# Performance work log

Hardware: AMD Instinct MI355X
Metric: run time of the kernel (lower is better)

Reference implementation:

```python
import jax, jax.numpy as jnp
import numpy as np

B, N, DEG = 128, 512, 16          # graphs, nodes/graph, avg degree
NB = B * N                        # 65536 nodes
E = NB * DEG                      # 1048576 edges
K1, K2, K3 = 410, 205, 103        # ceil(0.8*512), ceil(0.5*410), ceil(0.5*205)
H, C = 4, 32                      # GAT heads, head dim
F_IN, ED = 128, 7


def _glorot(key, shape, fan_in):
    return jax.random.normal(key, shape, dtype=jnp.float32) / np.float32(np.sqrt(fan_in))


def setup_inputs() -> dict:
    key = jax.random.key(0)
    ks = jax.random.split(key, 24)
    x = jax.random.normal(ks[0], (NB, F_IN), dtype=jnp.float32)
    # random intra-graph edges, then offset per graph
    src = jax.random.randint(ks[1], (E,), 0, N)
    dst = jax.random.randint(ks[2], (E,), 0, N)
    off = jnp.repeat(jnp.arange(B) * N, N * DEG)
    edge_index = jnp.stack([src + off, dst + off]).astype(jnp.int32)
    edge_attr = jax.random.normal(ks[3], (E, ED), dtype=jnp.float32)
    p = {
        'c1_wl': _glorot(ks[4], (F_IN, F_IN), F_IN), 'c1_bl': jnp.zeros((F_IN,), jnp.float32), 'c1_wr': _glorot(ks[5], (F_IN, F_IN), F_IN),
        'p1_w': _glorot(ks[6], (F_IN,), F_IN),
        'c2_wl': _glorot(ks[7], (F_IN, F_IN), F_IN), 'c2_bl': jnp.zeros((F_IN,), jnp.float32), 'c2_wr': _glorot(ks[8], (F_IN, F_IN), F_IN),
        'p2_wrel': _glorot(ks[9], (F_IN, 1), F_IN), 'p2_brel': jnp.zeros((1,), jnp.float32), 'p2_wroot': _glorot(ks[10], (F_IN, 1), F_IN),
        'g_w': _glorot(ks[11], (F_IN, H * C), F_IN), 'g_as': _glorot(ks[12], (H, C), C), 'g_ad': _glorot(ks[13], (H, C), C),
        'g_we': _glorot(ks[14], (ED, H * C), ED), 'g_ae': _glorot(ks[15], (H, C), C), 'g_b': jnp.zeros((H * C,), jnp.float32),
        'p3_wrel': _glorot(ks[16], (F_IN, 1), F_IN), 'p3_brel': jnp.zeros((1,), jnp.float32), 'p3_wroot': _glorot(ks[17], (F_IN, 1), F_IN),
        'l1_w': _glorot(ks[18], (F_IN, F_IN), F_IN), 'l1_b': jnp.zeros((F_IN,), jnp.float32),
        'l2_w': _glorot(ks[19], (F_IN, 64), F_IN), 'l2_b': jnp.zeros((64,), jnp.float32),
        'l3_w': _glorot(ks[20], (64, 1), 64), 'l3_b': jnp.zeros((1,), jnp.float32),
    }
    return {'x': x, 'edge_index': edge_index, 'edge_attr': edge_attr, **p}


def _sage(x, src, dst, emf, wl, bl, wr):
    # SAGEConv: mean-aggregate neighbors (masked edges), lin_l(agg)+lin_r(x)
    agg = jax.ops.segment_sum(x[src] * emf[:, None], dst, num_segments=NB)
    cnt = jax.ops.segment_sum(emf, dst, num_segments=NB)
    mean = agg / jnp.maximum(cnt, 1.0)[:, None]
    return mean @ wl + bl + x @ wr


def _graphconv(x, src, dst, emf, wrel, brel, wroot):
    # GraphConv (SAGPooling score GNN): add-aggregation
    agg = jax.ops.segment_sum(x[src] * emf[:, None], dst, num_segments=NB)
    return (agg @ wrel + brel + x @ wroot).reshape(-1)


def _pool(x, score, nmask, K):
    # per-graph static top-k (equal-size graphs) == PyG topk + filter
    masked = jnp.where(nmask, score, -jnp.inf).reshape(B, N)
    idx = jax.lax.top_k(masked, K)[1]
    nm = jnp.zeros((B, N), dtype=bool).at[jnp.arange(B)[:, None], idx].set(True).reshape(-1)
    x = jnp.where(nm[:, None], x * score[:, None], 0.0)
    return x, nm


def _gap(x, K):
    # global mean pool; dropped nodes are exactly zero, K live nodes per graph
    return x.reshape(B, N, F_IN).sum(axis=1) / K


def _gat(x, src, dst, emf, nmask, edge_attr, w, a_s, a_d, w_e, a_e, b):
    xs = (x @ w).reshape(NB, H, C)
    al_s = (xs * a_s).sum(-1)                                   # [NB,H]
    al_d = (xs * a_d).sum(-1)
    al_e = ((edge_attr @ w_e).reshape(E, H, C) * a_e).sum(-1)    # [E,H]
    alpha = jax.nn.leaky_relu(al_s[src] + al_d[dst] + al_e, 0.2)
    alpha = jnp.where(emf[:, None] > 0, alpha, -jnp.inf)
    # PyG add_self_loops=True with fill_value='mean' for edge_attr
    ea_mean = (edge_attr * emf[:, None]).sum(0) / jnp.maximum(emf.sum(), 1.0)
    al_se = ((ea_mean @ w_e).reshape(H, C) * a_e).sum(-1)        # [H]
    alpha_self = jax.nn.leaky_relu(al_s + al_d + al_se[None, :], 0.2)
    alpha_self = jnp.where(nmask[:, None], alpha_self, -jnp.inf)
    m = jnp.maximum(jax.ops.segment_max(alpha, dst, num_segments=NB), alpha_self)
    m = jnp.where(jnp.isfinite(m), m, 0.0)
    ex = jnp.exp(alpha - m[dst]) * emf[:, None]
    ex_s = jnp.where(nmask[:, None], jnp.exp(alpha_self - m), 0.0)
    den = jnp.maximum(jax.ops.segment_sum(ex, dst, num_segments=NB) + ex_s, 1e-16)
    num = jax.ops.segment_sum(ex[:, :, None] * xs[src], dst, num_segments=NB) + ex_s[:, :, None] * xs
    return (num / den[:, :, None]).reshape(NB, H * C) + b


def _forward(x, edge_index, edge_attr, c1_wl, c1_bl, c1_wr, p1_w, c2_wl, c2_bl, c2_wr,
             p2_wrel, p2_brel, p2_wroot, g_w, g_as, g_ad, g_we, g_ae, g_b,
             p3_wrel, p3_brel, p3_wroot, l1_w, l1_b, l2_w, l2_b, l3_w, l3_b):
    src, dst = edge_index[0], edge_index[1]
    nmask = jnp.ones((NB,), dtype=bool)
    emf = jnp.ones((E,), jnp.float32)

    # block 1: SAGEConv -> TopKPooling(0.8) -> gap
    x = jax.nn.relu(_sage(x, src, dst, emf, c1_wl, c1_bl, c1_wr))
    s1 = jnp.tanh((x @ p1_w) / jnp.linalg.norm(p1_w))
    x, nmask = _pool(x, s1, nmask, K1)
    emf = emf * nmask[src] * nmask[dst]
    x1 = _gap(x, K1)

    # block 2: SAGEConv -> SAGPooling(0.5) -> gap
    x = jax.nn.relu(_sage(x, src, dst, emf, c2_wl, c2_bl, c2_wr))
    s2 = jnp.tanh(_graphconv(x, src, dst, emf, p2_wrel, p2_brel, p2_wroot))
    x, nmask = _pool(x, s2, nmask, K2)
    emf = emf * nmask[src] * nmask[dst]
    x2 = _gap(x, K2)

    # block 3: GATConv(128->32x4, edge_dim=7) -> SAGPooling(0.5) -> gap
    x = jax.nn.relu(_gat(x, src, dst, emf, nmask, edge_attr, g_w, g_as, g_ad, g_we, g_ae, g_b))
    s3 = jnp.tanh(_graphconv(x, src, dst, emf, p3_wrel, p3_brel, p3_wroot))
    x, nmask = _pool(x, s3, nmask, K3)
    x3 = _gap(x, K3)

    h = x1 + x2 + x3
    h = jax.nn.relu(h @ l1_w + l1_b)
    h = jax.nn.relu(h @ l2_w + l2_b)   # dropout identity in eval
    return jax.nn.sigmoid(h @ l3_w + l3_b)[:, 0]


def reference(x, edge_index, edge_attr, c1_wl, c1_bl, c1_wr, p1_w, c2_wl, c2_bl, c2_wr,
              p2_wrel, p2_brel, p2_wroot, g_w, g_as, g_ad, g_we, g_ae, g_b,
              p3_wrel, p3_brel, p3_wroot, l1_w, l1_b, l2_w, l2_b, l3_w, l3_b):
    return _forward(x, edge_index, edge_attr, c1_wl, c1_bl, c1_wr, p1_w, c2_wl, c2_bl, c2_wr,
                    p2_wrel, p2_brel, p2_wroot, g_w, g_as, g_ad, g_we, g_ae, g_b,
                    p3_wrel, p3_brel, p3_wroot, l1_w, l1_b, l2_w, l2_b, l3_w, l3_b)
```

## Files before the change

kernel.cpp:

```cpp
#include <hip/hip_runtime.h>
#include <math.h>

#define NBV 65536
#define EV  1048576
#define BV  128
#define K1V 410
#define K2V 205
#define K3V 103
#define NL2 (BV*K2V)
#define NEG_BIG (-1.0e38f)

__device__ __forceinline__ float lrelu(float x){ return x > 0.f ? x : 0.2f*x; }

__global__ void k_init1(float* nmask, int* dcnt, int* fill, float* out, float sval){
  int i = blockIdx.x*blockDim.x + threadIdx.x;
  if (i < 128) out[i] = sval;
  if (i < NBV) nmask[i] = 1.f;
  if (i < NBV+1){ dcnt[i] = 0; fill[i] = 0; }
}

__global__ void k_hist(const int* dst, int* dcnt){
  int e = blockIdx.x*blockDim.x + threadIdx.x;
  if (e < EV) atomicAdd(&dcnt[dst[e]], 1);
}

__global__ void k_scan1(const int* dcnt, int* rp, int* bsum){
  __shared__ int sc[256];
  int t = threadIdx.x, i = blockIdx.x*256 + t;
  int v = dcnt[i];
  sc[t] = v; __syncthreads();
  for (int o = 1; o < 256; o <<= 1){
    int x = (t >= o) ? sc[t-o] : 0;
    __syncthreads();
    sc[t] += x;
    __syncthreads();
  }
  rp[i] = sc[t];
  if (t == 255) bsum[blockIdx.x] = sc[t];
}

__global__ void k_scan2(int* bsum){
  __shared__ int sc[256];
  int t = threadIdx.x;
  int v = bsum[t];
  sc[t] = v; __syncthreads();
  for (int o = 1; o < 256; o <<= 1){
    int x = (t >= o) ? sc[t-o] : 0;
    __syncthreads();
    sc[t] += x;
    __syncthreads();
  }
  bsum[t] = sc[t] - v;
}

__global__ void k_scan3(int* rp, const int* dcnt, const int* bsum){
  int t = threadIdx.x, i = blockIdx.x*256 + t;
  rp[i] = rp[i] - dcnt[i] + bsum[blockIdx.x];
  if (i == 0) rp[NBV] = EV;
}

__global__ void k_scatter(const int* src, const int* dst, const int* rp, int* fill,
                          int* csr_src, int* csr_eid){
  int e = blockIdx.x*blockDim.x + threadIdx.x;
  if (e < EV){
    int d = dst[e];
    int pos = atomicAdd(&fill[d], 1);
    int slot = rp[d] + pos;
    csr_src[slot] = src[e];
    csr_eid[slot] = e;
  }
}

__global__ void k_ve_inv(const float* g_we, const float* g_ae, const float* p1w, float* sml){
  __shared__ float sc[128];
  int t = threadIdx.x;
  if (t < 28){
    int ed = t >> 2, h = t & 3;
    float a = 0.f;
    for (int c = 0; c < 32; c++) a += g_we[ed*128 + h*32 + c] * g_ae[h*32 + c];
    sml[20 + t] = a;
  }
  float v = p1w[t];
  sc[t] = v*v; __syncthreads();
  for (int o = 64; o > 0; o >>= 1){ if (t < o) sc[t] += sc[t+o]; __syncthreads(); }
  if (t == 0) sml[0] = 1.f / sqrtf(sc[0]);
}

__global__ void k_ale(const float* ea, const float* ve, float* ALE){
  int e = blockIdx.x*blockDim.x + threadIdx.x;
  if (e < EV){
    float a0=0.f,a1=0.f,a2=0.f,a3=0.f;
    for (int ed = 0; ed < 7; ed++){
      float x = ea[e*7 + ed];
      a0 += x*ve[ed*4+0]; a1 += x*ve[ed*4+1]; a2 += x*ve[ed*4+2]; a3 += x*ve[ed*4+3];
    }
    float4 o; o.x=a0; o.y=a1; o.z=a2; o.w=a3;
    *(float4*)&ALE[(size_t)e*4] = o;
  }
}

__global__ void __launch_bounds__(256) k_sage_agg(const float* X, const float* nmask,
    const int* rp, const int* csr_src, float* AGG, int masked,
    const int* nidx, int kper){
  int g = blockIdx.x & 127;
  int blk = blockIdx.x >> 7;
  int r = blk*8 + (threadIdx.x >> 5);
  int i;
  if (nidx){ if (r >= kper) return; i = nidx[g*kper + r]; }
  else i = g*512 + r;
  int c4 = threadIdx.x & 31;
  float ax=0.f,ay=0.f,az=0.f,aw=0.f,cnt=0.f;
  if (!masked || nmask[i] > 0.f){
    int r0 = rp[i], r1 = rp[i+1];
    int s = r0;
    for (; s + 4 <= r1; s += 4){
      int sn0 = csr_src[s+0], sn1 = csr_src[s+1], sn2 = csr_src[s+2], sn3 = csr_src[s+3];
      float nm0 = masked ? nmask[sn0] : 1.f;
      float nm1 = masked ? nmask[sn1] : 1.f;
      float nm2 = masked ? nmask[sn2] : 1.f;
      float nm3 = masked ? nmask[sn3] : 1.f;
      if (nm0 > 0.f){ float4 v = *(const float4*)&X[((size_t)sn0 << 7) + (c4 << 2)];
                      ax += v.x; ay += v.y; az += v.z; aw += v.w; cnt += 1.f; }
      if (nm1 > 0.f){ float4 v = *(const float4*)&X[((size_t)sn1 << 7) + (c4 << 2)];
                      ax += v.x; ay += v.y; az += v.z; aw += v.w; cnt += 1.f; }
      if (nm2 > 0.f){ float4 v = *(const float4*)&X[((size_t)sn2 << 7) + (c4 << 2)];
                      ax += v.x; ay += v.y; az += v.z; aw += v.w; cnt += 1.f; }
      if (nm3 > 0.f){ float4 v = *(const float4*)&X[((size_t)sn3 << 7) + (c4 << 2)];
                      ax += v.x; ay += v.y; az += v.z; aw += v.w; cnt += 1.f; }
    }
    for (; s < r1; s++){
      int sn = csr_src[s];
      float nm = masked ? nmask[sn] : 1.f;
      if (nm > 0.f){
        const float4 v = *(const float4*)&X[((size_t)sn << 7) + (c4 << 2)];
        ax += v.x; ay += v.y; az += v.z; aw += v.w; cnt += 1.f;
      }
    }
  }
  float inv = 1.f / fmaxf(cnt, 1.f);
  float4 o; o.x = ax*inv; o.y = ay*inv; o.z = az*inv; o.w = aw*inv;
  *(float4*)&AGG[((size_t)i << 7) + (c4 << 2)] = o;
}

__global__ void __launch_bounds__(512) k_gemm(const float* A1, const float* A2,
    const float* W1, const float* W2, const float* bias,
    float* OUT, int has2, int relu, int hasb,
    const int* ridx, int sc_mode,
    const float* sw1, const float* sw2, const float* sinv,
    float* so1, float* so2){
  __shared__ float ws[128][128];
  __shared__ float as[16][136];
  int t = threadIdx.x;
  int n0 = blockIdx.x * 128;
  int rowg = t >> 5;
  int colg = t & 31;
  int rb = rowg * 8;
  int jb = colg * 4;
  int an = t >> 2;
  int ak = (t & 3) << 2;
  int arow = ridx ? ridx[n0 + an] : (n0 + an);
  float acc[8][4];
  for (int r = 0; r < 8; r++)
    for (int j = 0; j < 4; j++) acc[r][j] = 0.f;
  int nmat = has2 ? 2 : 1;
  for (int m = 0; m < nmat; m++){
    const float* A = (m == 0) ? A1 : A2;
    const float* W = (m == 0) ? W1 : W2;
    __syncthreads();
    for (int ii = 0; ii < 8; ii++){
      int idx4 = t + 512*ii;
      int kk = idx4 >> 5;
      int jj = (idx4 & 31) << 2;
      *(float4*)&ws[kk][jj] = *(const float4*)&W[kk*128 + jj];
    }
    float4 rA = *(const float4*)&A[((size_t)arow << 7) + ak];
    for (int c = 0; c < 8; c++){
      if (c > 0) __syncthreads();
      as[ak+0][an] = rA.x;
      as[ak+1][an] = rA.y;
      as[ak+2][an] = rA.z;
      as[ak+3][an] = rA.w;
      __syncthreads();
      if (c+1 < 8)
        rA = *(const float4*)&A[((size_t)arow << 7) + (c+1)*16 + ak];
      int kb = c*16;
      for (int kk = 0; kk < 16; kk++){
        float4 wv = *(const float4*)&ws[kb+kk][jb];
        float4 aL = *(const float4*)&as[kk][rb];
        float4 aH = *(const float4*)&as[kk][rb+4];
        float a0=aL.x,a1=aL.y,a2=aL.z,a3=aL.w,a4=aH.x,a5=aH.y,a6=aH.z,a7=aH.w;
        acc[0][0]+=a0*wv.x; acc[0][1]+=a0*wv.y; acc[0][2]+=a0*wv.z; acc[0][3]+=a0*wv.w;
        acc[1][0]+=a1*wv.x; acc[1][1]+=a1*wv.y; acc[1][2]+=a1*wv.z; acc[1][3]+=a1*wv.w;
        acc[2][0]+=a2*wv.x; acc[2][1]+=a2*wv.y; acc[2][2]+=a2*wv.z; acc[2][3]+=a2*wv.w;
        acc[3][0]+=a3*wv.x; acc[3][1]+=a3*wv.y; acc[3][2]+=a3*wv.z; acc[3][3]+=a3*wv.w;
        acc[4][0]+=a4*wv.x; acc[4][1]+=a4*wv.y; acc[4][2]+=a4*wv.z; acc[4][3]+=a4*wv.w;
        acc[5][0]+=a5*wv.x; acc[5][1]+=a5*wv.y; acc[5][2]+=a5*wv.z; acc[5][3]+=a5*wv.w;
        acc[6][0]+=a6*wv.x; acc[6][1]+=a6*wv.y; acc[6][2]+=a6*wv.z; acc[6][3]+=a6*wv.w;
        acc[7][0]+=a7*wv.x; acc[7][1]+=a7*wv.y; acc[7][2]+=a7*wv.z; acc[7][3]+=a7*wv.w;
      }
    }
  }
  float bj0=0.f,bj1=0.f,bj2=0.f,bj3=0.f;
  if (hasb){
    bj0 = bias[jb+0]; bj1 = bias[jb+1]; bj2 = bias[jb+2]; bj3 = bias[jb+3];
  }
  int orow[8];
  for (int r = 0; r < 8; r++) orow[r] = ridx ? ridx[n0+rb+r] : (n0+rb+r);
  float w1x=0.f,w1y=0.f,w1z=0.f,w1w=0.f, w2x=0.f,w2y=0.f,w2z=0.f,w2w=0.f;
  if (sc_mode){
    float4 t1 = *(const float4*)&sw1[jb];
    w1x=t1.x; w1y=t1.y; w1z=t1.z; w1w=t1.w;
    if (sc_mode >= 2){
      float4 t2 = *(const float4*)&sw2[jb];
      w2x=t2.x; w2y=t2.y; w2z=t2.z; w2w=t2.w;
    }
  }
  float pd1[8], pd2[8];
  for (int r = 0; r < 8; r++){
    float4 o;
    o.x = acc[r][0]+bj0; o.y = acc[r][1]+bj1; o.z = acc[r][2]+bj2; o.w = acc[r][3]+bj3;
    if (relu){
      o.x = fmaxf(o.x,0.f); o.y = fmaxf(o.y,0.f); o.z = fmaxf(o.z,0.f); o.w = fmaxf(o.w,0.f);
    }
    if (sc_mode){
      pd1[r] = o.x*w1x + o.y*w1y + o.z*w1z + o.w*w1w;
      if (sc_mode >= 2) pd2[r] = o.x*w2x + o.y*w2y + o.z*w2z + o.w*w2w;
    }
    *(float4*)&OUT[((size_t)orow[r] << 7) + jb] = o;
  }
  if (sc_mode == 1){
    float inv = sinv[0];
    for (int r = 0; r < 8; r++){
      float a = pd1[r];
      for (int o = 16; o > 0; o >>= 1) a += __shfl_down(a, o, 32);
      if (colg == 0) so1[orow[r]] = tanhf(a * inv);
    }
  } else if (sc_mode == 2){
    for (int r = 0; r < 8; r++){
      float a = pd1[r];
      float b = pd2[r];
      for (int o = 16; o > 0; o >>= 1){
        a += __shfl_down(a, o, 32);
        b += __shfl_down(b, o, 32);
      }
      if (colg == 0){ so1[orow[r]] = a; so2[orow[r]] = b; }
    }
  } else if (sc_mode == 3){
    int base = colg & ~7;
    for (int r = 0; r < 8; r++){
      float s1 = 0.f, s2 = 0.f;
      for (int c4 = 0; c4 < 8; c4++){
        s1 += __shfl(pd1[r], base + c4, 32);
        s2 += __shfl(pd2[r], base + c4, 32);
      }
      if ((colg & 7) == 0){
        int h = colg >> 3;
        so1[orow[r]*4 + h] = s1;
        so2[orow[r]*4 + h] = s2;
      }
    }
  }
}

__global__ void k_gconv(const float* q, const float* r, const float* nmask,
    const int* rp, const int* csr_src, const float* brel, float* s){
  int i = blockIdx.x*blockDim.x + threadIdx.x;
  if (i >= NBV) return;
  float acc = 0.f;
  if (nmask[i] > 0.f){
    int r0 = rp[i], r1 = rp[i+1];
    int t2 = r0;
    for (; t2 + 4 <= r1; t2 += 4){
      int sn0 = csr_src[t2+0], sn1 = csr_src[t2+1], sn2 = csr_src[t2+2], sn3 = csr_src[t2+3];
      float nm0 = nmask[sn0], nm1 = nmask[sn1], nm2 = nmask[sn2], nm3 = nmask[sn3];
      if (nm0 > 0.f) acc += q[sn0];
      if (nm1 > 0.f) acc += q[sn1];
      if (nm2 > 0.f) acc += q[sn2];
      if (nm3 > 0.f) acc += q[sn3];
    }
    for (; t2 < r1; t2++){
      int sn = csr_src[t2];
      if (nmask[sn] > 0.f) acc += q[sn];
    }
  }
  s[i] = tanhf(acc + brel[0] + r[i]);
}

__global__ void __launch_bounds__(512) k_poolscale(const float* s, float* nmask,
    float* X, float* gap, int K, int* cidx, float invK){
  __shared__ float sc[512];
  __shared__ float lsel[512];
  __shared__ float prt[8][128];
  int b = blockIdx.x, t = threadIdx.x;
  int i = b*512 + t;
  float nm = nmask[i];
  float sv = s[i];
  float ms = (nm > 0.f) ? sv : NEG_BIG;
  sc[t] = ms;
  __syncthreads();
  int rank = 0;
  for (int j = 0; j < 512; j++){
    float o = sc[j];
    rank += ((o > ms) || (o == ms && j < t)) ? 1 : 0;
  }
  bool selb = rank < K;
  nmask[i] = selb ? 1.f : 0.f;
  if (cidx && selb) cidx[b*K + rank] = i;
  __syncthreads();
  sc[t] = selb ? 1.f : 0.f;
  lsel[t] = selb ? sv : 0.f;
  __syncthreads();
  int c = t & 127, g = t >> 7;
  for (int qq = 0; qq < 2; qq++){
    int q = g*2 + qq;
    float acc = 0.f;
    for (int n = q*64; n < q*64 + 64; n++){
      if (sc[n] > 0.f){
        size_t idx = (((size_t)(b*512 + n)) << 7) + c;
        float v = X[idx] * lsel[n];
        X[idx] = v;
        acc += v;
      }
    }
    prt[q][c] = acc;
  }
  __syncthreads();
  if (t < 128){
    float ss = 0.f;
    for (int q = 0; q < 8; q++) ss += prt[q][t];
    gap[b*128 + t] = ss * invK;
  }
}

__global__ void __launch_bounds__(256) k_ea_part(const float* ea, const int* srcA, const int* dstA,
    const float* nmask, float* part){
  float p[8] = {0.f,0.f,0.f,0.f,0.f,0.f,0.f,0.f};
  for (int e = blockIdx.x*256 + threadIdx.x; e < EV; e += 256*256){
    if (nmask[srcA[e]] > 0.f && nmask[dstA[e]] > 0.f){
      for (int d = 0; d < 7; d++) p[d] += ea[e*7 + d];
      p[7] += 1.f;
    }
  }
  __shared__ float red[256];
  for (int comp = 0; comp < 8; comp++){
    red[threadIdx.x] = p[comp]; __syncthreads();
    for (int o = 128; o > 0; o >>= 1){ if (threadIdx.x < o) red[threadIdx.x] += red[threadIdx.x + o]; __syncthreads(); }
    if (threadIdx.x == 0) part[blockIdx.x*8 + comp] = red[0];
    __syncthreads();
  }
}

__global__ void k_ea_fin(const float* part, const float* ve, float* alse){
  __shared__ float es[8];
  int h = threadIdx.x;
  if (h < 8){
    float s = 0.f;
    for (int b = 0; b < 256; b++) s += part[b*8 + h];
    es[h] = s;
  }
  __syncthreads();
  if (h == 0){
    float cnt = fmaxf(es[7], 1.f);
    for (int hh = 0; hh < 4; hh++){
      float s = 0.f;
      for (int ed = 0; ed < 7; ed++) s += (es[ed]/cnt) * ve[ed*4 + hh];
      alse[hh] = s;
    }
  }
}

__global__ void __launch_bounds__(256) k_gat(const float* xs, const float* alS, const float* alD,
    const float* ALE, const float* nmask, const int* rp, const int* csr_src,
    const int* csr_eid, const float* alse, const float* g_b,
    const float* wrel, const float* wroot, const int* nidx, int kper,
    float* qv, float* rv, float* OUT){
  int g = blockIdx.x & 127;
  int blk = blockIdx.x >> 7;
  int r = blk*8 + (threadIdx.x >> 5);
  int i;
  if (nidx){ if (r >= kper) return; i = nidx[g*kper + r]; }
  else i = g*512 + r;
  int lane = threadIdx.x & 31;
  int h = lane >> 3;
  int ch = h*8 + (lane & 7);
  float nmi = nmask[i];
  const float4* xs4 = (const float4*)xs;
  float m = 0.f, den = 0.f;
  float4 acc; acc.x=0.f; acc.y=0.f; acc.z=0.f; acc.w=0.f;
  if (nmi > 0.f){
    float ald_i = alD[i*4 + h];
    m = lrelu(alS[i*4 + h] + ald_i + alse[h]);
    den = 1.f;
    acc = xs4[(size_t)i*32 + ch];
    int r0 = rp[i], r1 = rp[i+1];
    int s = r0;
    for (; s + 4 <= r1; s += 4){
      int sn0 = csr_src[s+0], sn1 = csr_src[s+1], sn2 = csr_src[s+2], sn3 = csr_src[s+3];
      float nm0 = nmask[sn0], nm1 = nmask[sn1], nm2 = nmask[sn2], nm3 = nmask[sn3];
      if (nm0 > 0.f){
        float a = lrelu(alS[sn0*4 + h] + ald_i + ALE[(size_t)csr_eid[s+0]*4 + h]);
        float4 v = xs4[(size_t)sn0*32 + ch];
        float mn = fmaxf(m, a); float pm = expf(m - mn); float pa = expf(a - mn);
        den = den*pm + pa;
        acc.x = acc.x*pm + pa*v.x; acc.y = acc.y*pm + pa*v.y;
        acc.z = acc.z*pm + pa*v.z; acc.w = acc.w*pm + pa*v.w;
        m = mn;
      }
      if (nm1 > 0.f){
        float a = lrelu(alS[sn1*4 + h] + ald_i + ALE[(size_t)csr_eid[s+1]*4 + h]);
        float4 v = xs4[(size_t)sn1*32 + ch];
        float mn = fmaxf(m, a); float pm = expf(m - mn); float pa = expf(a - mn);
        den = den*pm + pa;
        acc.x = acc.x*pm + pa*v.x; acc.y = acc.y*pm + pa*v.y;
        acc.z = acc.z*pm + pa*v.z; acc.w = acc.w*pm + pa*v.w;
        m = mn;
      }
      if (nm2 > 0.f){
        float a = lrelu(alS[sn2*4 + h] + ald_i + ALE[(size_t)csr_eid[s+2]*4 + h]);
        float4 v = xs4[(size_t)sn2*32 + ch];
        float mn = fmaxf(m, a); float pm = expf(m - mn); float pa = expf(a - mn);
        den = den*pm + pa;
        acc.x = acc.x*pm + pa*v.x; acc.y = acc.y*pm + pa*v.y;
        acc.z = acc.z*pm + pa*v.z; acc.w = acc.w*pm + pa*v.w;
        m = mn;
      }
      if (nm3 > 0.f){
        float a = lrelu(alS[sn3*4 + h] + ald_i + ALE[(size_t)csr_eid[s+3]*4 + h]);
        float4 v = xs4[(size_t)sn3*32 + ch];
        float mn = fmaxf(m, a); float pm = expf(m - mn); float pa = expf(a - mn);
        den = den*pm + pa;
        acc.x = acc.x*pm + pa*v.x; acc.y = acc.y*pm + pa*v.y;
        acc.z = acc.z*pm + pa*v.z; acc.w = acc.w*pm + pa*v.w;
        m = mn;
      }
    }
    for (; s < r1; s++){
      int sn = csr_src[s];
      if (nmask[sn] > 0.f){
        float a = lrelu(alS[sn*4 + h] + ald_i + ALE[(size_t)csr_eid[s]*4 + h]);
        float4 v = xs4[(size_t)sn*32 + ch];
        float mn = fmaxf(m, a); float pm = expf(m - mn); float pa = expf(a - mn);
        den = den*pm + pa;
        acc.x = acc.x*pm + pa*v.x; acc.y = acc.y*pm + pa*v.y;
        acc.z = acc.z*pm + pa*v.z; acc.w = acc.w*pm + pa*v.w;
        m = mn;
      }
    }
  }
  den = fmaxf(den, 1e-16f);
  float rd = 1.f/den;
  int cb = ch << 2;
  float4 o;
  o.x = fmaxf(acc.x*rd + g_b[cb+0], 0.f);
  o.y = fmaxf(acc.y*rd + g_b[cb+1], 0.f);
  o.z = fmaxf(acc.z*rd + g_b[cb+2], 0.f);
  o.w = fmaxf(acc.w*rd + g_b[cb+3], 0.f);
  *(float4*)&OUT[((size_t)i << 7) + cb] = o;
  float4 wa = *(const float4*)&wrel[cb];
  float4 wb = *(const float4*)&wroot[cb];
  float aq = o.x*wa.x + o.y*wa.y + o.z*wa.z + o.w*wa.w;
  float ar = o.x*wb.x + o.y*wb.y + o.z*wb.z + o.w*wb.w;
  for (int off = 16; off > 0; off >>= 1){
    aq += __shfl_down(aq, off, 32);
    ar += __shfl_down(ar, off, 32);
  }
  if (lane == 0){ qv[i] = aq; rv[i] = ar; }
}

__global__ void __launch_bounds__(128) k_mlp(const float* x1g, const float* x2g, const float* x3g,
    const float* l1w, const float* l1b, const float* l2w, const float* l2b,
    const float* l3w, const float* l3b, float* out){
  __shared__ float hh[128];
  __shared__ float h2[128];
  __shared__ float h3[64];
  int b = blockIdx.x, t = threadIdx.x;
  hh[t] = x1g[b*128 + t] + x2g[b*128 + t] + x3g[b*128 + t];
  __syncthreads();
  float a = l1b[t];
  for (int k = 0; k < 128; k++) a += hh[k] * l1w[k*128 + t];
  h2[t] = fmaxf(a, 0.f);
  __syncthreads();
  if (t < 64){
    float a2 = l2b[t];
    for (int k = 0; k < 128; k++) a2 += h2[k] * l2w[k*64 + t];
    h3[t] = fmaxf(a2, 0.f);
  }
  __syncthreads();
  if (t == 0){
    float z = l3b[0];
    for (int k = 0; k < 64; k++) z += h3[k] * l3w[k];
    out[b] = 1.f/(1.f + expf(-z));
  }
}

extern "C" void kernel_launch(void* const* d_in, const int* in_sizes, int n_in,
                              void* d_out, int out_size, void* d_ws, size_t ws_size,
                              hipStream_t stream){
  const float* x       = (const float*)d_in[0];
  const int*   ei      = (const int*)d_in[1];
  const float* ea      = (const float*)d_in[2];
  const float* c1_wl   = (const float*)d_in[3];
  const float* c1_bl   = (const float*)d_in[4];
  const float* c1_wr   = (const float*)d_in[5];
  const float* p1_w    = (const float*)d_in[6];
  const float* c2_wl   = (const float*)d_in[7];
  const float* c2_bl   = (const float*)d_in[8];
  const float* c2_wr   = (const float*)d_in[9];
  const float* p2_wrel = (const float*)d_in[10];
  const float* p2_brel = (const float*)d_in[11];
  const float* p2_wroot= (const float*)d_in[12];
  const float* g_w     = (const float*)d_in[13];
  const float* g_as    = (const float*)d_in[14];
  const float* g_ad    = (const float*)d_in[15];
  const float* g_we    = (const float*)d_in[16];
  const float* g_ae    = (const float*)d_in[17];
  const float* g_b     = (const float*)d_in[18];
  const float* p3_wrel = (const float*)d_in[19];
  const float* p3_brel = (const float*)d_in[20];
  const float* p3_wroot= (const float*)d_in[21];
  const float* l1_w    = (const float*)d_in[22];
  const float* l1_b    = (const float*)d_in[23];
  const float* l2_w    = (const float*)d_in[24];
  const float* l2_b    = (const float*)d_in[25];
  const float* l3_w    = (const float*)d_in[26];
  const float* l3_b    = (const float*)d_in[27];
  float* out = (float*)d_out;
  (void)in_sizes; (void)n_in; (void)out_size;

  char* w = (char*)d_ws;
  size_t off = 0;
  float* AGG  = (float*)(w + off); off += (size_t)NBV*128*4;
  float* F1   = (float*)(w + off); off += (size_t)NBV*128*4;
  float* F2   = (float*)(w + off); off += (size_t)NBV*128*4;
  float* ALE  = (float*)(w + off); off += (size_t)EV*4*4;
  float* sA   = (float*)(w + off); off += (size_t)NBV*4;
  float* qv   = (float*)(w + off); off += (size_t)NBV*4;
  float* rv   = (float*)(w + off); off += (size_t)NBV*4;
  float* nmask= (float*)(w + off); off += (size_t)NBV*4;
  float* alS  = (float*)(w + off); off += (size_t)NBV*4*4;
  float* alD  = (float*)(w + off); off += (size_t)NBV*4*4;
  float* x1g  = (float*)(w + off); off += (size_t)BV*128*4;
  float* x2g  = (float*)(w + off); off += (size_t)BV*128*4;
  float* x3g  = (float*)(w + off); off += (size_t)BV*128*4;
  float* sml  = (float*)(w + off); off += 64*4;
  float* eprt = (float*)(w + off); off += 2048*4;
  int* csr_src = (int*)(w + off); off += (size_t)EV*4;
  int* csr_eid = (int*)(w + off); off += (size_t)EV*4;
  int* rp      = (int*)(w + off); off += (size_t)(NBV+64)*4;
  int* dcnt    = (int*)(w + off); off += (size_t)(NBV+64)*4;
  int* fill    = (int*)(w + off); off += (size_t)(NBV+64)*4;
  int* cidx1   = (int*)(w + off); off += (size_t)NBV*4;
  int* cidx2   = (int*)(w + off); off += (size_t)NBV*4;
  int* bsum    = (int*)(w + off); off += 1024;
  size_t needed = off;

  float sentinel = (ws_size >= needed) ? 0.125f : 0.875f;

  const int* srcA = ei;
  const int* dstA = ei + EV;

  k_init1<<<(NBV+256)/256, 256, 0, stream>>>(nmask, dcnt, fill, out, sentinel);
  k_hist<<<EV/256, 256, 0, stream>>>(dstA, dcnt);
  k_scan1<<<256, 256, 0, stream>>>(dcnt, rp, bsum);
  k_scan2<<<1, 256, 0, stream>>>(bsum);
  k_scan3<<<256, 256, 0, stream>>>(rp, dcnt, bsum);
  k_scatter<<<EV/256, 256, 0, stream>>>(srcA, dstA, rp, fill, csr_src, csr_eid);
  k_ve_inv<<<1, 128, 0, stream>>>(g_we, g_ae, p1_w, sml);
  k_ale<<<EV/256, 256, 0, stream>>>(ea, sml+20, ALE);

  k_sage_agg<<<(NBV*32)/256, 256, 0, stream>>>(x, nmask, rp, csr_src, AGG, 0,
                                               (const int*)nullptr, 512);
  k_gemm<<<NBV/128, 512, 0, stream>>>(AGG, x, c1_wl, c1_wr, c1_bl, F1, 1, 1, 1,
                                      (const int*)nullptr, 1, p1_w, (const float*)nullptr, sml, sA, (float*)nullptr);
  k_poolscale<<<BV, 512, 0, stream>>>(sA, nmask, F1, x1g, K1V, cidx1, 1.f/(float)K1V);

  k_sage_agg<<<BV*52, 256, 0, stream>>>(F1, nmask, rp, csr_src, AGG, 1, cidx1, K1V);
  k_gemm<<<NBV/128, 512, 0, stream>>>(AGG, F1, c2_wl, c2_wr, c2_bl, F2, 1, 1, 1,
                                      (const int*)nullptr, 2, p2_wrel, p2_wroot, (const float*)nullptr, qv, rv);
  k_gconv<<<NBV/256, 256, 0, stream>>>(qv, rv, nmask, rp, csr_src, p2_brel, sA);
  k_poolscale<<<BV, 512, 0, stream>>>(sA, nmask, F2, x2g, K2V, cidx2, 1.f/(float)K2V);

  k_gemm<<<NL2/128, 512, 0, stream>>>(F2, F2, g_w, g_w, g_b, AGG, 0, 0, 0,
                                      cidx2, 3, g_as, g_ad,
                                      (const float*)nullptr, alS, alD);
  k_ea_part<<<256, 256, 0, stream>>>(ea, srcA, dstA, nmask, eprt);
  k_ea_fin<<<1, 64, 0, stream>>>(eprt, sml+20, sml+16);
  k_gat<<<BV*26, 256, 0, stream>>>(AGG, alS, alD, ALE, nmask, rp, csr_src, csr_eid,
                                   sml+16, g_b, p3_wrel, p3_wroot, cidx2, K2V, qv, rv, F1);
  k_gconv<<<NBV/256, 256, 0, stream>>>(qv, rv, nmask, rp, csr_src, p3_brel, sA);
  k_poolscale<<<BV, 512, 0, stream>>>(sA, nmask, F1, x3g, K3V, (int*)nullptr, 1.f/(float)K3V);

  k_mlp<<<BV, 128, 0, stream>>>(x1g, x2g, x3g, l1_w, l1_b, l2_w, l2_b, l3_w, l3_b, out);
}
```

Measured before the change: 674.8 us.

## Fuse SAGE neighbor mean aggregation into the GEMM A-tile loader

New measurement: 872.5 us. 1.29x slower.

```diff
diff --git a/kernel.cpp b/kernel.cpp
--- a/kernel.cpp
+++ b/kernel.cpp
@@ -99,55 +99,13 @@
   }
 }
 
-__global__ void __launch_bounds__(256) k_sage_agg(const float* X, const float* nmask,
-    const int* rp, const int* csr_src, float* AGG, int masked,
-    const int* nidx, int kper){
-  int g = blockIdx.x & 127;
-  int blk = blockIdx.x >> 7;
-  int r = blk*8 + (threadIdx.x >> 5);
-  int i;
-  if (nidx){ if (r >= kper) return; i = nidx[g*kper + r]; }
-  else i = g*512 + r;
-  int c4 = threadIdx.x & 31;
-  float ax=0.f,ay=0.f,az=0.f,aw=0.f,cnt=0.f;
-  if (!masked || nmask[i] > 0.f){
-    int r0 = rp[i], r1 = rp[i+1];
-    int s = r0;
-    for (; s + 4 <= r1; s += 4){
-      int sn0 = csr_src[s+0], sn1 = csr_src[s+1], sn2 = csr_src[s+2], sn3 = csr_src[s+3];
-      float nm0 = masked ? nmask[sn0] : 1.f;
-      float nm1 = masked ? nmask[sn1] : 1.f;
-      float nm2 = masked ? nmask[sn2] : 1.f;
-      float nm3 = masked ? nmask[sn3] : 1.f;
-      if (nm0 > 0.f){ float4 v = *(const float4*)&X[((size_t)sn0 << 7) + (c4 << 2)];
-                      ax += v.x; ay += v.y; az += v.z; aw += v.w; cnt += 1.f; }
-      if (nm1 > 0.f){ float4 v = *(const float4*)&X[((size_t)sn1 << 7) + (c4 << 2)];
-                      ax += v.x; ay += v.y; az += v.z; aw += v.w; cnt += 1.f; }
-      if (nm2 > 0.f){ float4 v = *(const float4*)&X[((size_t)sn2 << 7) + (c4 << 2)];
-                      ax += v.x; ay += v.y; az += v.z; aw += v.w; cnt += 1.f; }
-      if (nm3 > 0.f){ float4 v = *(const float4*)&X[((size_t)sn3 << 7) + (c4 << 2)];
-                      ax += v.x; ay += v.y; az += v.z; aw += v.w; cnt += 1.f; }
-    }
-    for (; s < r1; s++){
-      int sn = csr_src[s];
-      float nm = masked ? nmask[sn] : 1.f;
-      if (nm > 0.f){
-        const float4 v = *(const float4*)&X[((size_t)sn << 7) + (c4 << 2)];
-        ax += v.x; ay += v.y; az += v.z; aw += v.w; cnt += 1.f;
-      }
-    }
-  }
-  float inv = 1.f / fmaxf(cnt, 1.f);
-  float4 o; o.x = ax*inv; o.y = ay*inv; o.z = az*inv; o.w = aw*inv;
-  *(float4*)&AGG[((size_t)i << 7) + (c4 << 2)] = o;
-}
-
 __global__ void __launch_bounds__(512) k_gemm(const float* A1, const float* A2,
     const float* W1, const float* W2, const float* bias,
     float* OUT, int has2, int relu, int hasb,
     const int* ridx, int sc_mode,
     const float* sw1, const float* sw2, const float* sinv,
-    float* so1, float* so2){
+    float* so1, float* so2,
+    int agg_mode, const float* nmask, const int* rp, const int* csr_src){
   __shared__ float ws[128][128];
   __shared__ float as[16][136];
   int t = threadIdx.x;
@@ -166,6 +124,7 @@
   for (int m = 0; m < nmat; m++){
     const float* A = (m == 0) ? A1 : A2;
     const float* W = (m == 0) ? W1 : W2;
+    bool agg = (m == 0) && (agg_mode != 0);
     __syncthreads();
     for (int ii = 0; ii < 8; ii++){
       int idx4 = t + 512*ii;
@@ -173,16 +132,60 @@
       int jj = (idx4 & 31) << 2;
       *(float4*)&ws[kk][jj] = *(const float4*)&W[kk*128 + jj];
     }
-    float4 rA = *(const float4*)&A[((size_t)arow << 7) + ak];
+    float4 rA;
+    float ax=0.f, ay=0.f, az=0.f, aw=0.f, invn = 1.f;
+    int nr0 = 0, nr1 = 0;
+    bool rowlive = true;
+    if (agg){
+      nr0 = rp[arow]; nr1 = rp[arow+1];
+      if (agg_mode == 2 && !(nmask[arow] > 0.f)) rowlive = false;
+      float cnt = 0.f;
+      if (rowlive){
+        for (int s2 = nr0; s2 < nr1; s2++){
+          int sn = csr_src[s2];
+          float nm = (agg_mode == 2) ? nmask[sn] : 1.f;
+          if (nm > 0.f){
+            float4 v = *(const float4*)&A[((size_t)sn << 7) + ak];
+            ax += v.x; ay += v.y; az += v.z; aw += v.w; cnt += 1.f;
+          }
+        }
+      }
+      invn = 1.f / fmaxf(cnt, 1.f);
+    } else {
+      rA = *(const float4*)&A[((size_t)arow << 7) + ak];
+    }
     for (int c = 0; c < 8; c++){
       if (c > 0) __syncthreads();
-      as[ak+0][an] = rA.x;
-      as[ak+1][an] = rA.y;
-      as[ak+2][an] = rA.z;
-      as[ak+3][an] = rA.w;
+      if (agg){
+        as[ak+0][an] = ax*invn;
+        as[ak+1][an] = ay*invn;
+        as[ak+2][an] = az*invn;
+        as[ak+3][an] = aw*invn;
+      } else {
+        as[ak+0][an] = rA.x;
+        as[ak+1][an] = rA.y;
+        as[ak+2][an] = rA.z;
+        as[ak+3][an] = rA.w;
+      }
       __syncthreads();
-      if (c+1 < 8)
-        rA = *(const float4*)&A[((size_t)arow << 7) + (c+1)*16 + ak];
+      if (c+1 < 8){
+        if (agg){
+          ax = ay = az = aw = 0.f;
+          if (rowlive){
+            int kb2 = (c+1)*16 + ak;
+            for (int s2 = nr0; s2 < nr1; s2++){
+              int sn = csr_src[s2];
+              float nm = (agg_mode == 2) ? nmask[sn] : 1.f;
+              if (nm > 0.f){
+                float4 v = *(const float4*)&A[((size_t)sn << 7) + kb2];
+                ax += v.x; ay += v.y; az += v.z; aw += v.w;
+              }
+            }
+          }
+        } else {
+          rA = *(const float4*)&A[((size_t)arow << 7) + (c+1)*16 + ak];
+        }
+      }
       int kb = c*16;
       for (int kk = 0; kk < 16; kk++){
         float4 wv = *(const float4*)&ws[kb+kk][jb];
@@ -568,21 +571,21 @@
   k_ve_inv<<<1, 128, 0, stream>>>(g_we, g_ae, p1_w, sml);
   k_ale<<<EV/256, 256, 0, stream>>>(ea, sml+20, ALE);
 
-  k_sage_agg<<<(NBV*32)/256, 256, 0, stream>>>(x, nmask, rp, csr_src, AGG, 0,
-                                               (const int*)nullptr, 512);
-  k_gemm<<<NBV/128, 512, 0, stream>>>(AGG, x, c1_wl, c1_wr, c1_bl, F1, 1, 1, 1,
-                                      (const int*)nullptr, 1, p1_w, (const float*)nullptr, sml, sA, (float*)nullptr);
+  k_gemm<<<NBV/128, 512, 0, stream>>>(x, x, c1_wl, c1_wr, c1_bl, F1, 1, 1, 1,
+                                      (const int*)nullptr, 1, p1_w, (const float*)nullptr, sml, sA, (float*)nullptr,
+                                      1, nmask, rp, csr_src);
   k_poolscale<<<BV, 512, 0, stream>>>(sA, nmask, F1, x1g, K1V, cidx1, 1.f/(float)K1V);
 
-  k_sage_agg<<<BV*52, 256, 0, stream>>>(F1, nmask, rp, csr_src, AGG, 1, cidx1, K1V);
-  k_gemm<<<NBV/128, 512, 0, stream>>>(AGG, F1, c2_wl, c2_wr, c2_bl, F2, 1, 1, 1,
-                                      (const int*)nullptr, 2, p2_wrel, p2_wroot, (const float*)nullptr, qv, rv);
+  k_gemm<<<NBV/128, 512, 0, stream>>>(F1, F1, c2_wl, c2_wr, c2_bl, F2, 1, 1, 1,
+                                      (const int*)nullptr, 2, p2_wrel, p2_wroot, (const float*)nullptr, qv, rv,
+                                      2, nmask, rp, csr_src);
   k_gconv<<<NBV/256, 256, 0, stream>>>(qv, rv, nmask, rp, csr_src, p2_brel, sA);
   k_poolscale<<<BV, 512, 0, stream>>>(sA, nmask, F2, x2g, K2V, cidx2, 1.f/(float)K2V);
 
   k_gemm<<<NL2/128, 512, 0, stream>>>(F2, F2, g_w, g_w, g_b, AGG, 0, 0, 0,
                                       cidx2, 3, g_as, g_ad,
-                                      (const float*)nullptr, alS, alD);
+                                      (const float*)nullptr, alS, alD,
+                                      0, (const float*)nullptr, (const int*)nullptr, (const int*)nullptr);
   k_ea_part<<<256, 256, 0, stream>>>(ea, srcA, dstA, nmask, eprt);
   k_ea_fin<<<1, 64, 0, stream>>>(eprt, sml+20, sml+16);
   k_gat<<<BV*26, 256, 0, stream>>>(AGG, alS, alD, ALE, nmask, rp, csr_src, csr_eid,
```
